# Performance work log

Hardware: AMD Instinct MI355X
Metric: run time of the kernel (lower is better)

Reference implementation:

```python
import jax, jax.numpy as jnp
import numpy as np
from jax import lax

B, C, H, W = 4, 32, 224, 224
KH, KW = 5, 5
KK = KH * KW
L = H * W


def setup_inputs() -> dict:
    key = jax.random.key(0)
    k1, k2, k3, k4 = jax.random.split(key, 4)
    return {
        "input_tensor": jax.random.normal(k1, (B, C, H, W), dtype=jnp.float32),
        "color_distance_tensor": jax.random.uniform(k2, (B, L, KK), dtype=jnp.float32),
        "color_weight": jax.random.uniform(k3, (1,), dtype=jnp.float32, minval=-0.005, maxval=0.005),
        "position_weight": jax.random.uniform(k4, (1,), dtype=jnp.float32, minval=-0.005, maxval=0.005),
    }


def reference(input_tensor, color_distance_tensor, color_weight, position_weight):
    kh, kw = KH, KW
    # torch F.pad(pad=(a,b,c,d)) pads LAST dim (width) with (a,b) and 2nd-last (height) with (c,d).
    # The source passes (kh//2,(kh-1)//2, kw//2,(kw-1)//2) -> width padded by kh-based, height by kw-based.
    pw_l, pw_r = kh // 2, (kh - 1) // 2
    ph_t, ph_b = kw // 2, (kw - 1) // 2
    padded = jnp.pad(input_tensor, ((0, 0), (0, 0), (ph_t, ph_b), (pw_l, pw_r)))
    # im2col: features ordered (C, kh, kw) like torch.nn.Unfold -> (B, C*KK, H, W)
    patches = lax.conv_general_dilated_patches(padded, (kh, kw), (1, 1), "VALID")
    unf = patches.reshape(B, C * KK, L).transpose(0, 2, 1)  # (B, L, C*KK)
    # replicate torch's reshape of the non-contiguous permuted tensor (index scramble):
    unf = unf.reshape(B, C, KK, L).transpose(0, 1, 3, 2)  # (B, C, L, KK)
    # position distances: (height_pos - kh//2)^2 (1,kh) + (width_pos - kw//2)^2 transposed (kw,1)
    hd = (jnp.arange(kh) - kh // 2) ** 2
    wd = (jnp.arange(kw) - kw // 2) ** 2
    pos = (hd[None, :] + wd[:, None]).reshape(-1).astype(jnp.float32)  # (KK,)
    weights = pos * position_weight + color_distance_tensor * color_weight  # (B, L, KK)
    weights = weights[:, None]  # (B, 1, L, KK) == torch unsqueeze(dim=1)
    out = (unf * weights).sum(-1).reshape(B, C, H, W)
    return out * input_tensor
```

## Files before the change

kernel.cpp:

```cpp
#include <hip/hip_runtime.h>

#define BB 4
#define CC 32
#define LL 50176
#define KK2 25
#define CDTOT (BB * LL * KK2)


__global__ __launch_bounds__(256) void conv_local_kernel(
    const float* __restrict__ input,
    const float* __restrict__ cd,
    const float* __restrict__ colw,
    const float* __restrict__ posw,
    float* __restrict__ out)
{
    __shared__ float smem[64 * 101 + 8];

    const int t    = threadIdx.x;
    const int lane = t & 63;
    const int w    = t >> 6;

    const int bx   = blockIdx.x;
    const int xcd  = bx & 7;
    const int slot = bx >> 3;
    const int b    = xcd >> 1;
    const int j    = slot * 2 + (xcd & 1);
    const int chunk  = j & 1;
    const int rem0   = (j >> 1) * 4;
    const int c2base = chunk * 16;

    const float cw = colw[0];
    const float pw = posw[0];
    const float* __restrict__ in_b  = input + b * (CC * LL);
    float* __restrict__       out_b = out   + b * (CC * LL);

    {
        const int cd_base = b * (LL * KK2);
        #pragma unroll
        for (int jld = 0; jld < 25; ++jld) {
            int flat = t + 256 * jld;
            int ci   = flat / 100;
            int pos  = flat - ci * 100;
            int gidx = cd_base + (rem0 + 800 * ci) * KK2 + pos;
            gidx = min(gidx, CDTOT - 1);
            smem[ci * 101 + pos] = __builtin_nontemporal_load(&cd[gidx]);
        }
    }
    __syncthreads();

    const int remU = __builtin_amdgcn_readfirstlane(rem0 + w);
    const int ii   = lane;

    int   A[KK2];
    float Wt[KK2];
    const float POS[KK2] = {8,5,4,5,8, 5,2,1,2,5, 4,1,0,1,4, 5,2,1,2,5, 8,5,4,5,8};

    #pragma unroll
    for (int k2 = 0; k2 < KK2; ++k2) {
        int t1 = 576 * k2 + remU;
        int q0 = t1 / 800;
        int r  = t1 - q0 * 800;
        int c  = r / 25;
        int s  = r - c * 25;
        int dy = s / 5 - 2;
        int dx = s % 5 - 2;
        int u  = 62 * k2 + q0 + ii;
        int ys = u / 224;
        int xs = u - ys * 224;
        int xm = xs + dx;
        bool xok = (unsigned)xm < 224u;
        int xc = min(max(xm, 0), 223);
        float wgt = fmaf(smem[ii * 101 + w * 25 + k2], cw, POS[k2] * pw);
        Wt[k2] = xok ? wgt : 0.0f;
        A[k2]  = c * LL + (ys + dy) * 224 + xc + c2base * 1568;
    }
    __syncthreads();

    const int remB = t & 3;
    const int iiB  = t >> 2;
    const int l2B  = rem0 + remB + 800 * iiB;
    const bool okB = l2B < LL;
    const int idxB = min(l2B, LL - 1);

    #pragma unroll 1
    for (int gg = 0; gg < 4; ++gg) {
        float acc[4];
        float iv[4];
        int   oidx[4];
        #pragma unroll
        for (int g = 0; g < 4; ++g) {
            oidx[g] = (c2base + gg * 4 + g) * LL + idxB;
            iv[g]   = in_b[oidx[g]];
        }
        #pragma unroll
        for (int g = 0; g < 4; ++g) {
            const int jj = gg * 4 + g;
            const bool sp0  = (chunk == 0) && (jj == 0);
            const bool sp31 = (chunk == 1) && (jj == 15);
            float a = 0.0f;
            if (sp0 | sp31) {
                #pragma unroll
                for (int k2 = 0; k2 < KK2; ++k2) {
                    int t1 = 576 * k2 + remU;
                    int q0 = t1 / 800;
                    int r  = t1 - q0 * 800;
                    int c  = r / 25;
                    int s  = r - c * 25;
                    int dy = s / 5 - 2;
                    int dx = s % 5 - 2;
                    int u  = 62 * k2 + q0 + ii;
                    int ys = u / 224;
                    int xs = u - ys * 224;
                    int xc = min(max(xs + dx, 0), 223);
                    int yy = ys + dy;
                    int yb = sp0 ? max(yy, 0) : (217 + min(yy, 6));
                    bool ok = sp0 ? (yy >= 0) : (yy <= 6);
                    float v = in_b[c * LL + yb * 224 + xc];
                    a = fmaf(ok ? v : 0.0f, Wt[k2], a);
                }
            } else {
                const int ofs = jj * 1568;
                #pragma unroll
                for (int k2 = 0; k2 < KK2; ++k2)
                    a = fmaf(in_b[A[k2] + ofs], Wt[k2], a);
            }
            acc[g] = a;
        }

        float* sbuf = smem + (gg & 1) * 1040;
        #pragma unroll
        for (int g = 0; g < 4; ++g)
            sbuf[g * 260 + w * 65 + lane] = acc[g];
        __syncthreads();
        #pragma unroll
        for (int g = 0; g < 4; ++g) {
            float S = sbuf[g * 260 + remB * 65 + iiB];
            if (okB) __builtin_nontemporal_store(S * iv[g], &out_b[oidx[g]]);
        }
    }
}

extern "C" void kernel_launch(void* const* d_in, const int* in_sizes, int n_in,
                              void* d_out, int out_size, void* d_ws, size_t ws_size,
                              hipStream_t stream) {
    const float* input = (const float*)d_in[0];
    const float* cdist = (const float*)d_in[1];
    const float* cwp   = (const float*)d_in[2];
    const float* pwp   = (const float*)d_in[3];
    float* o = (float*)d_out;

    dim3 grid(1600);
    dim3 block(256);
    hipLaunchKernelGGL(conv_local_kernel, grid, block, 0, stream,
                       input, cdist, cwp, pwp, o);
}
```

Baseline: 164.2 us.

## Process eight channels per iteration with shared per-tap base addresses

```diff
diff --git a/kernel.cpp b/kernel.cpp
--- a/kernel.cpp
+++ b/kernel.cpp
@@ -51,8 +51,8 @@
     const int remU = __builtin_amdgcn_readfirstlane(rem0 + w);
     const int ii   = lane;
 
-    int   A[KK2];
     float Wt[KK2];
+    int   A0u[KK2];
     const float POS[KK2] = {8,5,4,5,8, 5,2,1,2,5, 4,1,0,1,4, 5,2,1,2,5, 8,5,4,5,8};
 
     #pragma unroll
@@ -64,15 +64,15 @@
         int s  = r - c * 25;
         int dy = s / 5 - 2;
         int dx = s % 5 - 2;
-        int u  = 62 * k2 + q0 + ii;
+        int e0 = 62 * k2 + q0;
+        A0u[k2] = c * LL + 224 * dy + dx + e0;
+        int u  = e0 + ii;
         int ys = u / 224;
         int xs = u - ys * 224;
         int xm = xs + dx;
         bool xok = (unsigned)xm < 224u;
-        int xc = min(max(xm, 0), 223);
         float wgt = fmaf(smem[ii * 101 + w * 25 + k2], cw, POS[k2] * pw);
         Wt[k2] = xok ? wgt : 0.0f;
-        A[k2]  = c * LL + (ys + dy) * 224 + xc + c2base * 1568;
     }
     __syncthreads();
 
@@ -83,59 +83,61 @@
     const int idxB = min(l2B, LL - 1);
 
     #pragma unroll 1
-    for (int gg = 0; gg < 4; ++gg) {
-        float acc[4];
-        float iv[4];
-        int   oidx[4];
+    for (int gg = 0; gg < 2; ++gg) {
+        float acc[8], iv[8];
         #pragma unroll
-        for (int g = 0; g < 4; ++g) {
-            oidx[g] = (c2base + gg * 4 + g) * LL + idxB;
-            iv[g]   = in_b[oidx[g]];
-        }
-        #pragma unroll
-        for (int g = 0; g < 4; ++g) {
-            const int jj = gg * 4 + g;
-            const bool sp0  = (chunk == 0) && (jj == 0);
-            const bool sp31 = (chunk == 1) && (jj == 15);
-            float a = 0.0f;
-            if (sp0 | sp31) {
-                #pragma unroll
-                for (int k2 = 0; k2 < KK2; ++k2) {
-                    int t1 = 576 * k2 + remU;
-                    int q0 = t1 / 800;
-                    int r  = t1 - q0 * 800;
-                    int c  = r / 25;
-                    int s  = r - c * 25;
-                    int dy = s / 5 - 2;
-                    int dx = s % 5 - 2;
-                    int u  = 62 * k2 + q0 + ii;
-                    int ys = u / 224;
-                    int xs = u - ys * 224;
-                    int xc = min(max(xs + dx, 0), 223);
-                    int yy = ys + dy;
-                    int yb = sp0 ? max(yy, 0) : (217 + min(yy, 6));
-                    bool ok = sp0 ? (yy >= 0) : (yy <= 6);
-                    float v = in_b[c * LL + yb * 224 + xc];
-                    a = fmaf(ok ? v : 0.0f, Wt[k2], a);
-                }
-            } else {
-                const int ofs = jj * 1568;
-                #pragma unroll
-                for (int k2 = 0; k2 < KK2; ++k2)
-                    a = fmaf(in_b[A[k2] + ofs], Wt[k2], a);
-            }
-            acc[g] = a;
+        for (int g = 0; g < 8; ++g) {
+            acc[g] = 0.0f;
+            iv[g]  = in_b[(c2base + gg * 8 + g) * LL + idxB];
         }
 
-        float* sbuf = smem + (gg & 1) * 1040;
         #pragma unroll
-        for (int g = 0; g < 4; ++g)
-            sbuf[g * 260 + w * 65 + lane] = acc[g];
+        for (int k2 = 0; k2 < KK2; ++k2) {
+            const float wv = Wt[k2];
+            #pragma unroll
+            for (int g = 0; g < 8; ++g) {
+                int c2  = c2base + gg * 8 + g;
+                int c2e = min(max(c2, 1), 30);
+                const float* bp = in_b + (A0u[k2] + 1568 * c2e);
+                acc[g] = fmaf(bp[ii], wv, acc[g]);
+            }
+        }
+
+        const bool sp_here = (chunk == 0) ? (gg == 0) : (gg == 1);
+        if (sp_here) {
+            const bool sp0 = (chunk == 0);
+            float a = 0.0f;
+            #pragma unroll
+            for (int k2 = 0; k2 < KK2; ++k2) {
+                int t1 = 576 * k2 + remU;
+                int q0 = t1 / 800;
+                int r  = t1 - q0 * 800;
+                int c  = r / 25;
+                int s  = r - c * 25;
+                int dy = s / 5 - 2;
+                int dx = s % 5 - 2;
+                int u  = 62 * k2 + q0 + ii;
+                int ys = u / 224;
+                int xs = u - ys * 224;
+                int xc = min(max(xs + dx, 0), 223);
+                int yy = ys + dy;
+                int yb = sp0 ? max(yy, 0) : (217 + min(yy, 6));
+                bool ok = sp0 ? (yy >= 0) : (yy <= 6);
+                float v = in_b[c * LL + yb * 224 + xc];
+                a = fmaf(ok ? v : 0.0f, Wt[k2], a);
+            }
+            if (sp0) acc[0] = a; else acc[7] = a;
+        }
+
+        float* sbuf = smem + gg * 2560;
+        #pragma unroll
+        for (int g = 0; g < 8; ++g)
+            sbuf[g * 320 + w * 80 + lane] = acc[g];
         __syncthreads();
         #pragma unroll
-        for (int g = 0; g < 4; ++g) {
-            float S = sbuf[g * 260 + remB * 65 + iiB];
-            if (okB) __builtin_nontemporal_store(S * iv[g], &out_b[oidx[g]]);
+        for (int g = 0; g < 8; ++g) {
+            float S = sbuf[g * 320 + remB * 80 + iiB];
+            if (okB) out_b[(c2base + gg * 8 + g) * LL + idxB] = S * iv[g];
         }
     }
 }
```

New measurement: 137.5 us. -16.2%, faster.
